# Kernel tuning notes

Hardware: AMD Instinct MI355X
Metric: run time of the kernel (lower is better)

Reference implementation:

```python
import jax, jax.numpy as jnp
import numpy as np

DIM = 2048
N_HEADS = 16
N_KV_HEADS = 4
HEAD_DIM = 128
SLIDING_WINDOW = 1024
ROPE_BASE = 10000.0


def _rotate_half(x):
    d = x.shape[-1] // 2
    return jnp.concatenate((-x[..., d:], x[..., :d]), axis=-1)


def _rope_cos_sin(T, dtype):
    inv_freq = 1.0 / (ROPE_BASE ** (jnp.arange(0, HEAD_DIM, 2, dtype=jnp.float32) / HEAD_DIM))
    t = jnp.arange(T, dtype=jnp.float32)
    freqs = jnp.outer(t, inv_freq)            # [T, HEAD_DIM//2]
    emb = jnp.concatenate((freqs, freqs), axis=-1)  # [T, HEAD_DIM]
    return jnp.cos(emb).astype(dtype), jnp.sin(emb).astype(dtype)


def setup_inputs() -> dict:
    key = jax.random.key(0)
    kx, kq, kk, kv, ko = jax.random.split(key, 5)
    s_in = 1.0 / np.sqrt(DIM)
    s_o = 1.0 / np.sqrt(N_HEADS * HEAD_DIM)
    return {
        "x": jax.random.normal(kx, (1, 4096, DIM), dtype=jnp.float32),
        "Wq": jax.random.normal(kq, (DIM, N_HEADS * HEAD_DIM), dtype=jnp.float32) * s_in,
        "Wk": jax.random.normal(kk, (DIM, N_KV_HEADS * HEAD_DIM), dtype=jnp.float32) * s_in,
        "Wv": jax.random.normal(kv, (DIM, N_KV_HEADS * HEAD_DIM), dtype=jnp.float32) * s_in,
        "Wo": jax.random.normal(ko, (N_HEADS * HEAD_DIM, DIM), dtype=jnp.float32) * s_o,
    }


def reference(x, Wq, Wk, Wv, Wo):
    B, T, C = x.shape
    # projections -> [B, H, T, D]
    q = (x @ Wq).reshape(B, T, N_HEADS, HEAD_DIM).transpose(0, 2, 1, 3)
    k = (x @ Wk).reshape(B, T, N_KV_HEADS, HEAD_DIM).transpose(0, 2, 1, 3)
    v = (x @ Wv).reshape(B, T, N_KV_HEADS, HEAD_DIM).transpose(0, 2, 1, 3)

    cos, sin = _rope_cos_sin(T, x.dtype)      # [T, D], broadcast over B, H
    q = q * cos + _rotate_half(q) * sin
    k = k * cos + _rotate_half(k) * sin

    # GQA: repeat kv heads (repeat_interleave over head axis)
    kv_rep = N_HEADS // N_KV_HEADS
    k = jnp.repeat(k, kv_rep, axis=1)
    v = jnp.repeat(v, kv_rep, axis=1)

    scale = 1.0 / np.sqrt(HEAD_DIM)
    att = jnp.einsum("bhqd,bhkd->bhqk", q, k) * scale  # [B, H, T, T]

    i = jnp.arange(T)[:, None]
    j = jnp.arange(T)[None, :]
    allowed = (j <= i) & ((i - j) < SLIDING_WINDOW)     # causal + sliding window
    att = jnp.where(allowed, att, -jnp.inf)
    att = jax.nn.softmax(att, axis=-1)

    y = jnp.einsum("bhqk,bhkd->bhqd", att, v)           # [B, H, T, D]
    y = y.transpose(0, 2, 1, 3).reshape(B, T, N_HEADS * HEAD_DIM)
    return y @ Wo
```

## Files before the change

### kernel.cpp

```cpp
#include <hip/hip_runtime.h>
#include <math.h>

typedef __bf16 bf16;
typedef __bf16 bf16x8 __attribute__((ext_vector_type(8)));
typedef __bf16 bf16x4 __attribute__((ext_vector_type(4)));
typedef float f32x4 __attribute__((ext_vector_type(4)));

__device__ __forceinline__ void ldg_lds16(const bf16* g, bf16* l) {
#if __has_builtin(__builtin_amdgcn_global_load_lds)
    __builtin_amdgcn_global_load_lds(
        (const __attribute__((address_space(1))) void*)g,
        (__attribute__((address_space(3))) void*)l, 16, 0, 0);
#else
    *(bf16x8*)l = *(const bf16x8*)g;
#endif
}

__global__ void cvt_x(const float* __restrict__ X, bf16* __restrict__ Xb, int total8)
{
    int idx = blockIdx.x * 256 + threadIdx.x;
    if (idx >= total8) return;
    const float* p = X + (size_t)idx * 8;
    f32x4 a = *reinterpret_cast<const f32x4*>(p);
    f32x4 b = *reinterpret_cast<const f32x4*>(p + 4);
    bf16x8 r;
    r[0] = (bf16)a[0]; r[1] = (bf16)a[1]; r[2] = (bf16)a[2]; r[3] = (bf16)a[3];
    r[4] = (bf16)b[0]; r[5] = (bf16)b[1]; r[6] = (bf16)b[2]; r[7] = (bf16)b[3];
    *reinterpret_cast<bf16x8*>(Xb + (size_t)idx * 8) = r;
}

__global__ void cvt_wt3(const float* __restrict__ Wq, const float* __restrict__ Wk,
                        const float* __restrict__ Wv, bf16* __restrict__ Wt)
{
    __shared__ float t[32][33];
    int bx = blockIdx.x;
    const float* W; int Ncols, nbase;
    if (bx < 64)      { W = Wq; Ncols = 2048; nbase = 0;    }
    else if (bx < 80) { W = Wk; Ncols = 512;  nbase = 2048; bx -= 64; }
    else              { W = Wv; Ncols = 512;  nbase = 2560; bx -= 80; }
    const int n0 = bx * 32, k0 = blockIdx.y * 32;
    const int x = threadIdx.x, y = threadIdx.y;
    #pragma unroll
    for (int i = 0; i < 4; ++i)
        t[y + 8 * i][x] = W[(size_t)(k0 + y + 8 * i) * Ncols + n0 + x];
    __syncthreads();
    #pragma unroll
    for (int i = 0; i < 4; ++i)
        Wt[(size_t)(nbase + n0 + y + 8 * i) * 2048 + k0 + x] = (bf16)t[x][y + 8 * i];
}

__global__ void cvt_wt(const float* __restrict__ W, bf16* __restrict__ Wt, int Ncols)
{
    __shared__ float t[32][33];
    const int n0 = blockIdx.x * 32, k0 = blockIdx.y * 32;
    const int x = threadIdx.x, y = threadIdx.y;
    #pragma unroll
    for (int i = 0; i < 4; ++i)
        t[y + 8 * i][x] = W[(size_t)(k0 + y + 8 * i) * Ncols + n0 + x];
    __syncthreads();
    #pragma unroll
    for (int i = 0; i < 4; ++i)
        Wt[(size_t)(n0 + y + 8 * i) * 2048 + k0 + x] = (bf16)t[x][y + 8 * i];
}

__global__ __launch_bounds__(512, 2) void gemm256_qkv(
    const bf16* __restrict__ A, const bf16* __restrict__ Bt,
    bf16* __restrict__ Qo, bf16* __restrict__ Ko, bf16* __restrict__ Vt,
    int K)
{
    __shared__ __align__(16) bf16 smem[2 * 32768];

    const int tid  = threadIdx.x;
    const int lane = tid & 63;
    const int wave = tid >> 6;
    const int quad = lane >> 4;
    const int l16  = lane & 15;
    const int wm   = wave >> 2;
    const int wn   = wave & 3;

    const int m0 = blockIdx.y * 256;
    const int n0 = blockIdx.x * 256;

    int offA[4], offB[4];
    #pragma unroll
    for (int p = 0; p < 4; ++p) {
        int u = p * 512 + tid;
        int row = u >> 3;
        int kc8 = (u & 7) ^ (row & 7);
        offA[p] = (m0 + row) * K + kc8 * 8;
        offB[p] = (n0 + row) * K + kc8 * 8;
    }
    const int dstoff = tid * 8;

    const int xv = (l16 & 7) << 4;
    const int c0 = ((quad * 16) ^ xv) >> 1;
    const int c1 = ((64 + quad * 16) ^ xv) >> 1;
    const int rA = (wm * 128 + l16) * 64;
    const int rB = (wn * 64 + l16) * 64;

    f32x4 acc[8][4] = {};
    const int NT = K >> 6;

    {
        bf16* d0 = smem;
        bf16* d1 = smem + 32768;
        #pragma unroll
        for (int p = 0; p < 4; ++p) {
            ldg_lds16(A  + offA[p], d0 + p * 4096 + dstoff);
            ldg_lds16(Bt + offB[p], d0 + 16384 + p * 4096 + dstoff);
        }
        #pragma unroll
        for (int p = 0; p < 4; ++p) {
            ldg_lds16(A  + offA[p] + 64, d1 + p * 4096 + dstoff);
            ldg_lds16(Bt + offB[p] + 64, d1 + 16384 + p * 4096 + dstoff);
        }
    }
    asm volatile("s_waitcnt vmcnt(8)" ::: "memory");
    __builtin_amdgcn_sched_barrier(0);
    __builtin_amdgcn_s_barrier();
    __builtin_amdgcn_sched_barrier(0);

    for (int t = 0; t < NT; ++t) {
        const bf16* As = smem + (t & 1) * 32768;
        const bf16* Bs = As + 16384;

        bf16x8 a0[8], b0[4];
        #pragma unroll
        for (int i = 0; i < 8; ++i)
            a0[i] = *(const bf16x8*)(As + rA + i * 1024 + c0);
        #pragma unroll
        for (int i = 0; i < 4; ++i)
            b0[i] = *(const bf16x8*)(Bs + rB + i * 1024 + c0);

        #pragma unroll
        for (int mi = 0; mi < 8; ++mi)
            #pragma unroll
            for (int ni = 0; ni < 4; ++ni)
                acc[mi][ni] = __builtin_amdgcn_mfma_f32_16x16x32_bf16(
                    a0[mi], b0[ni], acc[mi][ni], 0, 0, 0);

        bf16x8 a1[8], b1[4];
        #pragma unroll
        for (int i = 0; i < 8; ++i)
            a1[i] = *(const bf16x8*)(As + rA + i * 1024 + c1);
        #pragma unroll
        for (int i = 0; i < 4; ++i)
            b1[i] = *(const bf16x8*)(Bs + rB + i * 1024 + c1);

        asm volatile("s_waitcnt lgkmcnt(0)" ::: "memory");
        __builtin_amdgcn_sched_barrier(0);
        __builtin_amdgcn_s_barrier();
        __builtin_amdgcn_sched_barrier(0);

        if (t + 2 < NT) {
            bf16* d = smem + (t & 1) * 32768;
            const int koff = (t + 2) * 64;
            #pragma unroll
            for (int p = 0; p < 4; ++p) {
                ldg_lds16(A  + offA[p] + koff, d + p * 4096 + dstoff);
                ldg_lds16(Bt + offB[p] + koff, d + 16384 + p * 4096 + dstoff);
            }
        }

        __builtin_amdgcn_s_setprio(1);
        #pragma unroll
        for (int mi = 0; mi < 8; ++mi)
            #pragma unroll
            for (int ni = 0; ni < 4; ++ni)
                acc[mi][ni] = __builtin_amdgcn_mfma_f32_16x16x32_bf16(
                    a1[mi], b1[ni], acc[mi][ni], 0, 0, 0);
        __builtin_amdgcn_s_setprio(0);

        if (t + 2 < NT) {
            asm volatile("s_waitcnt vmcnt(8)" ::: "memory");
            __builtin_amdgcn_sched_barrier(0);
            __builtin_amdgcn_s_barrier();
            __builtin_amdgcn_sched_barrier(0);
        } else if (t == NT - 2) {
            asm volatile("s_waitcnt vmcnt(0)" ::: "memory");
            __builtin_amdgcn_sched_barrier(0);
            __builtin_amdgcn_s_barrier();
            __builtin_amdgcn_sched_barrier(0);
        }
    }

    #pragma unroll
    for (int mi = 0; mi < 8; ++mi) {
        #pragma unroll
        for (int ni = 0; ni < 4; ++ni) {
            const int row = m0 + wm * 128 + mi * 16 + quad * 4;
            const int col = n0 + wn * 64 + ni * 16 + l16;
            if (n0 < 2048) {
                #pragma unroll
                for (int r = 0; r < 4; ++r)
                    Qo[(size_t)(row + r) * 2048 + col] = (bf16)acc[mi][ni][r];
            } else if (n0 < 2560) {
                #pragma unroll
                for (int r = 0; r < 4; ++r)
                    Ko[(size_t)(row + r) * 512 + (col - 2048)] = (bf16)acc[mi][ni][r];
            } else {
                bf16x4 v;
                #pragma unroll
                for (int r = 0; r < 4; ++r) v[r] = (bf16)acc[mi][ni][r];
                *reinterpret_cast<bf16x4*>(&Vt[(size_t)(col - 2560) * 4096 + row]) = v;
            }
        }
    }
}

__global__ __launch_bounds__(512, 2) void gemm_out(
    const bf16* __restrict__ A, const bf16* __restrict__ Bt,
    float* __restrict__ C, int K)
{
    __shared__ __align__(16) bf16 smem[2 * 24576];

    const int tid  = threadIdx.x;
    const int lane = tid & 63;
    const int wave = tid >> 6;
    const int quad = lane >> 4;
    const int l16  = lane & 15;
    const int wm   = wave >> 1;
    const int wn   = wave & 1;

    const int m0 = blockIdx.y * 256;
    const int n0 = blockIdx.x * 128;

    int offA[4], offB[2];
    #pragma unroll
    for (int p = 0; p < 4; ++p) {
        int u = p * 512 + tid;
        int row = u >> 3;
        int kc8 = (u & 7) ^ (row & 7);
        offA[p] = (m0 + row) * K + kc8 * 8;
    }
    #pragma unroll
    for (int p = 0; p < 2; ++p) {
        int u = p * 512 + tid;
        int row = u >> 3;
        int kc8 = (u & 7) ^ (row & 7);
        offB[p] = (n0 + row) * K + kc8 * 8;
    }
    const int dstoff = tid * 8;

    const int xv = (l16 & 7) << 4;
    const int c0 = ((quad * 16) ^ xv) >> 1;
    const int c1 = ((64 + quad * 16) ^ xv) >> 1;
    const int rA = (wm * 64 + l16) * 64;
    const int rB = (wn * 64 + l16) * 64;

    f32x4 acc[4][4] = {};
    const int NT = K >> 6;

    auto stage = [&](int tt, int bsel) {
        bf16* as = smem + bsel * 24576;
        bf16* bs = as + 16384;
        const int koff = tt * 64;
        #pragma unroll
        for (int p = 0; p < 4; ++p)
            ldg_lds16(A + offA[p] + koff, as + p * 4096 + dstoff);
        #pragma unroll
        for (int p = 0; p < 2; ++p)
            ldg_lds16(Bt + offB[p] + koff, bs + p * 4096 + dstoff);
    };

    stage(0, 0);
    stage(1, 1);
    asm volatile("s_waitcnt vmcnt(6)" ::: "memory");
    __builtin_amdgcn_sched_barrier(0);
    __builtin_amdgcn_s_barrier();
    __builtin_amdgcn_sched_barrier(0);

    for (int t = 0; t < NT; ++t) {
        const bf16* As = smem + (t & 1) * 24576;
        const bf16* Bs = As + 16384;

        bf16x8 a0[4], b0[4];
        #pragma unroll
        for (int i = 0; i < 4; ++i)
            a0[i] = *(const bf16x8*)(As + rA + i * 1024 + c0);
        #pragma unroll
        for (int i = 0; i < 4; ++i)
            b0[i] = *(const bf16x8*)(Bs + rB + i * 1024 + c0);

        #pragma unroll
        for (int mi = 0; mi < 4; ++mi)
            #pragma unroll
            for (int ni = 0; ni < 4; ++ni)
                acc[mi][ni] = __builtin_amdgcn_mfma_f32_16x16x32_bf16(
                    a0[mi], b0[ni], acc[mi][ni], 0, 0, 0);

        bf16x8 a1[4], b1[4];
        #pragma unroll
        for (int i = 0; i < 4; ++i)
            a1[i] = *(const bf16x8*)(As + rA + i * 1024 + c1);
        #pragma unroll
        for (int i = 0; i < 4; ++i)
            b1[i] = *(const bf16x8*)(Bs + rB + i * 1024 + c1);

        asm volatile("s_waitcnt lgkmcnt(0)" ::: "memory");
        __builtin_amdgcn_sched_barrier(0);
        __builtin_amdgcn_s_barrier();
        __builtin_amdgcn_sched_barrier(0);

        if (t + 2 < NT) stage(t + 2, t & 1);

        __builtin_amdgcn_s_setprio(1);
        #pragma unroll
        for (int mi = 0; mi < 4; ++mi)
            #pragma unroll
            for (int ni = 0; ni < 4; ++ni)
                acc[mi][ni] = __builtin_amdgcn_mfma_f32_16x16x32_bf16(
                    a1[mi], b1[ni], acc[mi][ni], 0, 0, 0);
        __builtin_amdgcn_s_setprio(0);

        if (t + 2 < NT) {
            asm volatile("s_waitcnt vmcnt(6)" ::: "memory");
            __builtin_amdgcn_sched_barrier(0);
            __builtin_amdgcn_s_barrier();
            __builtin_amdgcn_sched_barrier(0);
        } else if (t == NT - 2) {
            asm volatile("s_waitcnt vmcnt(0)" ::: "memory");
            __builtin_amdgcn_sched_barrier(0);
            __builtin_amdgcn_s_barrier();
            __builtin_amdgcn_sched_barrier(0);
        }
    }

    #pragma unroll
    for (int mi = 0; mi < 4; ++mi) {
        #pragma unroll
        for (int ni = 0; ni < 4; ++ni) {
            const int row = m0 + wm * 64 + mi * 16 + quad * 4;
            const int col = n0 + wn * 64 + ni * 16 + l16;
            #pragma unroll
            for (int r = 0; r < 4; ++r)
                C[(size_t)(row + r) * 2048 + col] = acc[mi][ni][r];
        }
    }
}

__global__ void rope_k(bf16* __restrict__ Kb, int total)
{
    int idx = blockIdx.x * 256 + threadIdx.x;
    if (idx >= total) return;
    int j  = idx & 63;
    int th = idx >> 6;
    int t  = th >> 2;

    bf16* p = Kb + (size_t)th * 128;
    const float NEG_LN1E4_64 = -0.14391155806323211f;
    float inv_freq = expf(NEG_LN1E4_64 * (float)j);
    float ang = (float)t * inv_freq;
    float c = cosf(ang), s = sinf(ang);
    float q0 = (float)p[j], q1 = (float)p[j + 64];
    p[j]      = (bf16)(q0 * c - q1 * s);
    p[j + 64] = (bf16)(q1 * c + q0 * s);
}

__global__ __launch_bounds__(256) void attn_v9(
    const bf16* __restrict__ Q, const bf16* __restrict__ K,
    const bf16* __restrict__ Vt, bf16* __restrict__ Y)
{
    const float scale = 0.08838834764831845f;

    __shared__ __align__(16) bf16 Ks[2 * 64 * 128];
    __shared__ __align__(16) bf16 Vs[2 * 128 * 64];
    __shared__ __align__(16) bf16 Pl[4][16 * 64];

    const int tid  = threadIdx.x;
    const int lane = tid & 63;
    const int wave = tid >> 6;
    const int quad = lane >> 4;
    const int l16  = lane & 15;

    const int i0  = (gridDim.x - 1 - blockIdx.x) * 64;
    const int h   = blockIdx.y;
    const int kvh = h >> 2;
    const int q0  = i0 + wave * 16;
    bf16* Plw = Pl[wave];

    const int ks = (i0 >= 1024) ? (i0 - 1024) : 0;
    const int nsteps = (i0 + 64 - ks) >> 6;

    auto stage = [&](int tt, int bsel) {
        const int k0s = ks + tt * 64;
        bf16* kd = Ks + bsel * 8192;
        bf16* vd = Vs + bsel * 8192;
        #pragma unroll
        for (int p = 0; p < 4; ++p) {
            int u = p * 256 + tid;
            int kk = u >> 4, sc = u & 15;
            ldg_lds16(K + (size_t)(k0s + kk) * 512 + kvh * 128 + (sc ^ (kk & 15)) * 8,
                      kd + u * 8);
        }
        #pragma unroll
        for (int p = 0; p < 4; ++p) {
            int u = p * 256 + tid;
            int d = u >> 3, sc = u & 7;
            ldg_lds16(Vt + (size_t)(kvh * 128 + d) * 4096 + k0s + (sc ^ (d & 7)) * 8,
                      vd + u * 8);
        }
    };

    stage(0, 0);
    stage(1, 1);

    bf16x8 qf[4];
    {
        const bf16* qp = Q + (size_t)(q0 + l16) * 2048 + h * 128 + quad * 8;
        bf16x8 qr_[4];
        #pragma unroll
        for (int c = 0; c < 4; ++c)
            qr_[c] = *reinterpret_cast<const bf16x8*>(qp + c * 32);
        const float NEG_LN1E4_64 = -0.14391155806323211f;
        const float tf = (float)(q0 + l16);
        #pragma unroll
        for (int c = 0; c < 2; ++c) {
            #pragma unroll
            for (int i = 0; i < 8; ++i) {
                float inv_freq = expf(NEG_LN1E4_64 * (float)(c * 32 + quad * 8 + i));
                float ang = tf * inv_freq;
                float cs = cosf(ang), sn = sinf(ang);
                float a = (float)qr_[c][i], b = (float)qr_[c + 2][i];
                qf[c][i]     = (bf16)(a * cs - b * sn);
                qf[c + 2][i] = (bf16)(b * cs + a * sn);
            }
        }
    }

    f32x4 o[8] = {};
    float lsum[4] = {0.f, 0.f, 0.f, 0.f};

    asm volatile("s_waitcnt vmcnt(8)" ::: "memory");
    __builtin_amdgcn_sched_barrier(0);
    __builtin_amdgcn_s_barrier();
    __builtin_amdgcn_sched_barrier(0);

    for (int t = 0; t < nsteps; ++t) {
        const int b  = t & 1;
        const int k0 = ks + t * 64;
        const bf16* Kb = Ks + b * 8192;
        const bf16* Vb = Vs + b * 8192;

        f32x4 s[4];
        __builtin_amdgcn_s_setprio(1);
        #pragma unroll
        for (int kh = 0; kh < 4; ++kh) {
            const int kk = kh * 16 + l16;
            f32x4 sv = {};
            #pragma unroll
            for (int c = 0; c < 4; ++c) {
                bf16x8 kf = *reinterpret_cast<const bf16x8*>(
                    &Kb[kk * 128 + (((c * 4 + quad) ^ (kk & 15)) * 8)]);
                sv = __builtin_amdgcn_mfma_f32_16x16x32_bf16(qf[c], kf, sv, 0, 0, 0);
            }
            s[kh] = sv;
        }
        __builtin_amdgcn_s_setprio(0);

        const bool full = (k0 + 63 <= q0) && (q0 + 15 - k0 < 1024);
        if (full) {
            #pragma unroll
            for (int kh = 0; kh < 4; ++kh) {
                #pragma unroll
                for (int r = 0; r < 4; ++r) {
                    float pv = __expf(s[kh][r] * scale);
                    lsum[r] += pv;
                    const int row = quad * 4 + r;
                    const int idx = row * 64 +
                        ((((kh * 2 + (l16 >> 3)) ^ (row & 7)) << 3) | (l16 & 7));
                    Plw[idx] = (bf16)pv;
                }
            }
        } else {
            #pragma unroll
            for (int kh = 0; kh < 4; ++kh) {
                const int key = k0 + kh * 16 + l16;
                #pragma unroll
                for (int r = 0; r < 4; ++r) {
                    const int qrow = q0 + quad * 4 + r;
                    bool ok = (unsigned)(qrow - key) < 1024u;
                    float pv = ok ? __expf(s[kh][r] * scale) : 0.f;
                    lsum[r] += pv;
                    const int row = quad * 4 + r;
                    const int idx = row * 64 +
                        ((((kh * 2 + (l16 >> 3)) ^ (row & 7)) << 3) | (l16 & 7));
                    Plw[idx] = (bf16)pv;
                }
            }
        }

        bf16x8 pf0 = *reinterpret_cast<const bf16x8*>(
            &Plw[l16 * 64 + ((quad ^ (l16 & 7)) << 3)]);
        bf16x8 pf1 = *reinterpret_cast<const bf16x8*>(
            &Plw[l16 * 64 + (((4 + quad) ^ (l16 & 7)) << 3)]);
        __builtin_amdgcn_s_setprio(1);
        #pragma unroll
        for (int n = 0; n < 8; ++n) {
            const int d = n * 16 + l16;
            bf16x8 v0 = *reinterpret_cast<const bf16x8*>(
                &Vb[d * 64 + (((quad) ^ (d & 7)) * 8)]);
            bf16x8 v1 = *reinterpret_cast<const bf16x8*>(
                &Vb[d * 64 + (((4 + quad) ^ (d & 7)) * 8)]);
            o[n] = __builtin_amdgcn_mfma_f32_16x16x32_bf16(pf0, v0, o[n], 0, 0, 0);
            o[n] = __builtin_amdgcn_mfma_f32_16x16x32_bf16(pf1, v1, o[n], 0, 0, 0);
        }
        __builtin_amdgcn_s_setprio(0);

        asm volatile("s_waitcnt lgkmcnt(0)" ::: "memory");
        __builtin_amdgcn_sched_barrier(0);
        __builtin_amdgcn_s_barrier();
        __builtin_amdgcn_sched_barrier(0);

        if (t + 2 < nsteps) {
            stage(t + 2, b);
            asm volatile("s_waitcnt vmcnt(8)" ::: "memory");
        } else {
            asm volatile("s_waitcnt vmcnt(0)" ::: "memory");
        }
        __builtin_amdgcn_sched_barrier(0);
        __builtin_amdgcn_s_barrier();
        __builtin_amdgcn_sched_barrier(0);
    }

    #pragma unroll
    for (int r = 0; r < 4; ++r) {
        #pragma unroll
        for (int off = 1; off < 16; off <<= 1)
            lsum[r] += __shfl_xor(lsum[r], off, 64);
    }
    #pragma unroll
    for (int r = 0; r < 4; ++r) {
        int row = q0 + quad * 4 + r;
        float inv = (lsum[r] > 0.f) ? 1.f / lsum[r] : 0.f;
        #pragma unroll
        for (int n = 0; n < 8; ++n)
            Y[(size_t)row * 2048 + h * 128 + n * 16 + l16] = (bf16)(o[n][r] * inv);
    }
}

extern "C" void kernel_launch(void* const* d_in, const int* in_sizes, int n_in,
                              void* d_out, int out_size, void* d_ws, size_t ws_size,
                              hipStream_t stream)
{
    const float* x  = (const float*)d_in[0];
    const float* Wq = (const float*)d_in[1];
    const float* Wk = (const float*)d_in[2];
    const float* Wv = (const float*)d_in[3];
    const float* Wo = (const float*)d_in[4];
    float* out = (float*)d_out;

    const int T = 4096, DIM = 2048;

    char* po = (char*)d_out;
    bf16* Qb = (bf16*)(po);
    bf16* Kb = (bf16*)(po + (16u << 20));
    bf16* Vtb = (bf16*)(po + (20u << 20));

    char* ws = (char*)d_ws;
    bf16* xb    = (bf16*)(ws);
    bf16* Wqkvt = (bf16*)(ws + (16u << 20));
    bf16* Yb    = (bf16*)(ws);
    bf16* Wot   = (bf16*)(ws + (16u << 20));

    cvt_x<<<dim3(T * DIM / 8 / 256), 256, 0, stream>>>(x, xb, T * DIM / 8);

    dim3 tb(32, 8);
    cvt_wt3<<<dim3(96, 64), tb, 0, stream>>>(Wq, Wk, Wv, Wqkvt);

    gemm256_qkv<<<dim3(3072 / 256, T / 256), 512, 0, stream>>>(
        xb, Wqkvt, Qb, Kb, Vtb, DIM);

    cvt_wt<<<dim3(2048 / 32, 64), tb, 0, stream>>>(Wo, Wot, 2048);

    int ktot = T * 4 * 64;
    rope_k<<<(ktot + 255) / 256, 256, 0, stream>>>(Kb, ktot);

    attn_v9<<<dim3(T / 64, 16), 256, 0, stream>>>(Qb, Kb, Vtb, Yb);

    gemm_out<<<dim3(2048 / 128, T / 256), 512, 0, stream>>>(
        Yb, Wot, out, DIM);
}
```

Baseline: 289.1 us.

## Retile QKV GEMM to 256x192 and simplify attention P-tile layout

```diff
diff --git a/kernel.cpp b/kernel.cpp
--- a/kernel.cpp
+++ b/kernel.cpp
@@ -68,7 +68,7 @@
     bf16* __restrict__ Qo, bf16* __restrict__ Ko, bf16* __restrict__ Vt,
     int K)
 {
-    __shared__ __align__(16) bf16 smem[2 * 32768];
+    __shared__ __align__(16) bf16 smem[2 * 28672];
 
     const int tid  = threadIdx.x;
     const int lane = tid & 63;
@@ -79,15 +79,21 @@
     const int wn   = wave & 3;
 
     const int m0 = blockIdx.y * 256;
-    const int n0 = blockIdx.x * 256;
-
-    int offA[4], offB[4];
+    const int n0 = blockIdx.x * 192;
+
+    int offA[4], offB[3];
     #pragma unroll
     for (int p = 0; p < 4; ++p) {
         int u = p * 512 + tid;
         int row = u >> 3;
         int kc8 = (u & 7) ^ (row & 7);
         offA[p] = (m0 + row) * K + kc8 * 8;
+    }
+    #pragma unroll
+    for (int p = 0; p < 3; ++p) {
+        int u = p * 512 + tid;
+        int row = u >> 3;
+        int kc8 = (u & 7) ^ (row & 7);
         offB[p] = (n0 + row) * K + kc8 * 8;
     }
     const int dstoff = tid * 8;
@@ -96,55 +102,55 @@
     const int c0 = ((quad * 16) ^ xv) >> 1;
     const int c1 = ((64 + quad * 16) ^ xv) >> 1;
     const int rA = (wm * 128 + l16) * 64;
-    const int rB = (wn * 64 + l16) * 64;
-
-    f32x4 acc[8][4] = {};
+    const int rB = (wn * 48 + l16) * 64;
+
+    f32x4 acc[8][3] = {};
     const int NT = K >> 6;
 
-    {
-        bf16* d0 = smem;
-        bf16* d1 = smem + 32768;
-        #pragma unroll
-        for (int p = 0; p < 4; ++p) {
-            ldg_lds16(A  + offA[p], d0 + p * 4096 + dstoff);
-            ldg_lds16(Bt + offB[p], d0 + 16384 + p * 4096 + dstoff);
-        }
-        #pragma unroll
-        for (int p = 0; p < 4; ++p) {
-            ldg_lds16(A  + offA[p] + 64, d1 + p * 4096 + dstoff);
-            ldg_lds16(Bt + offB[p] + 64, d1 + 16384 + p * 4096 + dstoff);
-        }
-    }
-    asm volatile("s_waitcnt vmcnt(8)" ::: "memory");
+    auto stage = [&](int tt, int bsel) {
+        bf16* as = smem + bsel * 28672;
+        bf16* bs = as + 16384;
+        const int koff = tt * 64;
+        #pragma unroll
+        for (int p = 0; p < 4; ++p)
+            ldg_lds16(A + offA[p] + koff, as + p * 4096 + dstoff);
+        #pragma unroll
+        for (int p = 0; p < 3; ++p)
+            ldg_lds16(Bt + offB[p] + koff, bs + p * 4096 + dstoff);
+    };
+
+    stage(0, 0);
+    stage(1, 1);
+    asm volatile("s_waitcnt vmcnt(7)" ::: "memory");
     __builtin_amdgcn_sched_barrier(0);
     __builtin_amdgcn_s_barrier();
     __builtin_amdgcn_sched_barrier(0);
 
     for (int t = 0; t < NT; ++t) {
-        const bf16* As = smem + (t & 1) * 32768;
+        const bf16* As = smem + (t & 1) * 28672;
         const bf16* Bs = As + 16384;
 
-        bf16x8 a0[8], b0[4];
+        bf16x8 a0[8], b0[3];
         #pragma unroll
         for (int i = 0; i < 8; ++i)
             a0[i] = *(const bf16x8*)(As + rA + i * 1024 + c0);
         #pragma unroll
-        for (int i = 0; i < 4; ++i)
+        for (int i = 0; i < 3; ++i)
             b0[i] = *(const bf16x8*)(Bs + rB + i * 1024 + c0);
 
         #pragma unroll
         for (int mi = 0; mi < 8; ++mi)
             #pragma unroll
-            for (int ni = 0; ni < 4; ++ni)
+            for (int ni = 0; ni < 3; ++ni)
                 acc[mi][ni] = __builtin_amdgcn_mfma_f32_16x16x32_bf16(
                     a0[mi], b0[ni], acc[mi][ni], 0, 0, 0);
 
-        bf16x8 a1[8], b1[4];
+        bf16x8 a1[8], b1[3];
         #pragma unroll
         for (int i = 0; i < 8; ++i)
             a1[i] = *(const bf16x8*)(As + rA + i * 1024 + c1);
         #pragma unroll
-        for (int i = 0; i < 4; ++i)
+        for (int i = 0; i < 3; ++i)
             b1[i] = *(const bf16x8*)(Bs + rB + i * 1024 + c1);
 
         asm volatile("s_waitcnt lgkmcnt(0)" ::: "memory");
@@ -152,27 +158,19 @@
         __builtin_amdgcn_s_barrier();
         __builtin_amdgcn_sched_barrier(0);
 
-        if (t + 2 < NT) {
-            bf16* d = smem + (t & 1) * 32768;
-            const int koff = (t + 2) * 64;
-            #pragma unroll
-            for (int p = 0; p < 4; ++p) {
-                ldg_lds16(A  + offA[p] + koff, d + p * 4096 + dstoff);
-                ldg_lds16(Bt + offB[p] + koff, d + 16384 + p * 4096 + dstoff);
-            }
-        }
+        if (t + 2 < NT) stage(t + 2, t & 1);
 
         __builtin_amdgcn_s_setprio(1);
         #pragma unroll
         for (int mi = 0; mi < 8; ++mi)
             #pragma unroll
-            for (int ni = 0; ni < 4; ++ni)
+            for (int ni = 0; ni < 3; ++ni)
                 acc[mi][ni] = __builtin_amdgcn_mfma_f32_16x16x32_bf16(
                     a1[mi], b1[ni], acc[mi][ni], 0, 0, 0);
         __builtin_amdgcn_s_setprio(0);
 
         if (t + 2 < NT) {
-            asm volatile("s_waitcnt vmcnt(8)" ::: "memory");
+            asm volatile("s_waitcnt vmcnt(7)" ::: "memory");
             __builtin_amdgcn_sched_barrier(0);
             __builtin_amdgcn_s_barrier();
             __builtin_amdgcn_sched_barrier(0);
@@ -187,14 +185,15 @@
     #pragma unroll
     for (int mi = 0; mi < 8; ++mi) {
         #pragma unroll
-        for (int ni = 0; ni < 4; ++ni) {
+        for (int ni = 0; ni < 3; ++ni) {
             const int row = m0 + wm * 128 + mi * 16 + quad * 4;
-            const int col = n0 + wn * 64 + ni * 16 + l16;
-            if (n0 < 2048) {
+            const int col = n0 + wn * 48 + ni * 16 + l16;
+            const int cb  = n0 + wn * 48 + ni * 16;
+            if (cb < 2048) {
                 #pragma unroll
                 for (int r = 0; r < 4; ++r)
                     Qo[(size_t)(row + r) * 2048 + col] = (bf16)acc[mi][ni][r];
-            } else if (n0 < 2560) {
+            } else if (cb < 2560) {
                 #pragma unroll
                 for (int r = 0; r < 4; ++r)
                     Ko[(size_t)(row + r) * 512 + (col - 2048)] = (bf16)acc[mi][ni][r];
@@ -357,7 +356,7 @@
     p[j + 64] = (bf16)(q1 * c + q0 * s);
 }
 
-__global__ __launch_bounds__(256) void attn_v9(
+__global__ __launch_bounds__(256) void attn_v10(
     const bf16* __restrict__ Q, const bf16* __restrict__ K,
     const bf16* __restrict__ Vt, bf16* __restrict__ Y)
 {
@@ -365,7 +364,7 @@
 
     __shared__ __align__(16) bf16 Ks[2 * 64 * 128];
     __shared__ __align__(16) bf16 Vs[2 * 128 * 64];
-    __shared__ __align__(16) bf16 Pl[4][16 * 64];
+    __shared__ __align__(16) bf16 Pl[4][16 * 72];
 
     const int tid  = threadIdx.x;
     const int lane = tid & 63;
@@ -402,16 +401,19 @@
         }
     };
 
+    bf16x8 qr_[4];
+    {
+        const bf16* qp = Q + (size_t)(q0 + l16) * 2048 + h * 128 + quad * 8;
+        #pragma unroll
+        for (int c = 0; c < 4; ++c)
+            qr_[c] = *reinterpret_cast<const bf16x8*>(qp + c * 32);
+    }
+
     stage(0, 0);
     stage(1, 1);
 
     bf16x8 qf[4];
     {
-        const bf16* qp = Q + (size_t)(q0 + l16) * 2048 + h * 128 + quad * 8;
-        bf16x8 qr_[4];
-        #pragma unroll
-        for (int c = 0; c < 4; ++c)
-            qr_[c] = *reinterpret_cast<const bf16x8*>(qp + c * 32);
         const float NEG_LN1E4_64 = -0.14391155806323211f;
         const float tf = (float)(q0 + l16);
         #pragma unroll
@@ -458,42 +460,21 @@
         }
         __builtin_amdgcn_s_setprio(0);
 
-        const bool full = (k0 + 63 <= q0) && (q0 + 15 - k0 < 1024);
-        if (full) {
-            #pragma unroll
-            for (int kh = 0; kh < 4; ++kh) {
-                #pragma unroll
-                for (int r = 0; r < 4; ++r) {
-                    float pv = __expf(s[kh][r] * scale);
-                    lsum[r] += pv;
-                    const int row = quad * 4 + r;
-                    const int idx = row * 64 +
-                        ((((kh * 2 + (l16 >> 3)) ^ (row & 7)) << 3) | (l16 & 7));
-                    Plw[idx] = (bf16)pv;
-                }
+        #pragma unroll
+        for (int kh = 0; kh < 4; ++kh) {
+            const int key = k0 + kh * 16 + l16;
+            #pragma unroll
+            for (int r = 0; r < 4; ++r) {
+                const int qrow = q0 + quad * 4 + r;
+                bool ok = (unsigned)(qrow - key) < 1024u;
+                float pv = ok ? __expf(s[kh][r] * scale) : 0.f;
+                lsum[r] += pv;
+                Plw[(quad * 4 + r) * 72 + kh * 16 + l16] = (bf16)pv;
             }
-        } else {
-            #pragma unroll
-            for (int kh = 0; kh < 4; ++kh) {
-                const int key = k0 + kh * 16 + l16;
-                #pragma unroll
-                for (int r = 0; r < 4; ++r) {
-                    const int qrow = q0 + quad * 4 + r;
-                    bool ok = (unsigned)(qrow - key) < 1024u;
-                    float pv = ok ? __expf(s[kh][r] * scale) : 0.f;
-                    lsum[r] += pv;
-                    const int row = quad * 4 + r;
-                    const int idx = row * 64 +
-                        ((((kh * 2 + (l16 >> 3)) ^ (row & 7)) << 3) | (l16 & 7));
-                    Plw[idx] = (bf16)pv;
-                }
-            }
-        }
-
-        bf16x8 pf0 = *reinterpret_cast<const bf16x8*>(
-            &Plw[l16 * 64 + ((quad ^ (l16 & 7)) << 3)]);
-        bf16x8 pf1 = *reinterpret_cast<const bf16x8*>(
-            &Plw[l16 * 64 + (((4 + quad) ^ (l16 & 7)) << 3)]);
+        }
+
+        bf16x8 pf0 = *reinterpret_cast<const bf16x8*>(&Plw[l16 * 72 + quad * 8]);
+        bf16x8 pf1 = *reinterpret_cast<const bf16x8*>(&Plw[l16 * 72 + 32 + quad * 8]);
         __builtin_amdgcn_s_setprio(1);
         #pragma unroll
         for (int n = 0; n < 8; ++n) {
@@ -568,7 +549,7 @@
     dim3 tb(32, 8);
     cvt_wt3<<<dim3(96, 64), tb, 0, stream>>>(Wq, Wk, Wv, Wqkvt);
 
-    gemm256_qkv<<<dim3(3072 / 256, T / 256), 512, 0, stream>>>(
+    gemm256_qkv<<<dim3(3072 / 192, T / 256), 512, 0, stream>>>(
         xb, Wqkvt, Qb, Kb, Vtb, DIM);
 
     cvt_wt<<<dim3(2048 / 32, 64), tb, 0, stream>>>(Wo, Wot, 2048);
@@ -576,7 +557,7 @@
     int ktot = T * 4 * 64;
     rope_k<<<(ktot + 255) / 256, 256, 0, stream>>>(Kb, ktot);
 
-    attn_v9<<<dim3(T / 64, 16), 256, 0, stream>>>(Qb, Kb, Vtb, Yb);
+    attn_v10<<<dim3(T / 64, 16), 256, 0, stream>>>(Qb, Kb, Vtb, Yb);
 
     gemm_out<<<dim3(2048 / 128, T / 256), 512, 0, stream>>>(
         Yb, Wot, out, DIM);
```

After: 289.3 us. Within noise of the previous version (+0.0%).
